# Optimization experiments

Measured on AMD Instinct MI355X. Metric: run time of the kernel, lower is better.

## Reference

```python
import jax, jax.numpy as jnp
import numpy as np

# dims: B batch, LK observed times, LQ reference times, D input_dim (value dim = 2D),
# ET embed_time, H heads, NH nhidden, LAT latent_dim
B, LK, LQ, D, ET, H, NH, LAT = 4, 256, 128, 32, 128, 4, 128, 20
DK = ET // H


def setup_inputs() -> dict:
    key = jax.random.key(0)
    ks = jax.random.split(key, 16)
    s = 0.05
    vals = jax.random.normal(ks[0], (B, LK, D), jnp.float32)
    msk = (jax.random.uniform(ks[1], (B, LK, D)) < 0.7).astype(jnp.float32)
    x = jnp.concatenate([vals * msk, msk], axis=-1)          # (B,LK,2D)
    time_steps = jnp.sort(jax.random.uniform(ks[2], (B, LK), jnp.float32), axis=-1)
    q_ref = jnp.linspace(0.0, 1.0, LQ, dtype=jnp.float32)     # fixed reference times
    lin = lambda k, o, i: s * jax.random.normal(k, (o, i), jnp.float32)
    return dict(
        x=x, time_steps=time_steps, q_ref=q_ref,
        w_lin=lin(ks[3], 1, 1), b_lin=jnp.zeros((1,), jnp.float32),
        w_per=lin(ks[4], ET - 1, 1), b_per=jnp.zeros((ET - 1,), jnp.float32),
        wq=lin(ks[5], ET, ET), bq=jnp.zeros((ET,), jnp.float32),
        wk=lin(ks[6], ET, ET), bk=jnp.zeros((ET,), jnp.float32),
        wo=lin(ks[7], NH, 2 * D * H), bo=jnp.zeros((NH,), jnp.float32),
        wih_f=lin(ks[8], 3 * NH, NH), whh_f=lin(ks[9], 3 * NH, NH),
        bih_f=jnp.zeros((3 * NH,), jnp.float32), bhh_f=jnp.zeros((3 * NH,), jnp.float32),
        wih_b=lin(ks[10], 3 * NH, NH), whh_b=lin(ks[11], 3 * NH, NH),
        bih_b=jnp.zeros((3 * NH,), jnp.float32), bhh_b=jnp.zeros((3 * NH,), jnp.float32),
        w1=lin(ks[12], 50, 2 * NH), b1=jnp.zeros((50,), jnp.float32),
        w2=lin(ks[13], 2 * LAT, 50), b2=jnp.zeros((2 * LAT,), jnp.float32),
    )


def _time_emb(tt, w_lin, b_lin, w_per, b_per):
    # learn_time_embedding: [linear(t), sin(periodic(t))]
    tt = tt[..., None]
    out1 = tt @ w_lin.T + b_lin
    out2 = jnp.sin(tt @ w_per.T + b_per)
    return jnp.concatenate([out1, out2], axis=-1)  # (..., ET)


def _gru_dir(xs, wih, whh, bih, bhh, reverse):
    # xs: (T, B, F); torch GRU cell math
    h0 = jnp.zeros((xs.shape[1], whh.shape[1]), xs.dtype)
    def step(h, xt):
        gi = xt @ wih.T + bih
        gh = h @ whh.T + bhh
        ir, iz, inn = jnp.split(gi, 3, axis=-1)
        hr, hz, hn = jnp.split(gh, 3, axis=-1)
        r = jax.nn.sigmoid(ir + hr)
        z = jax.nn.sigmoid(iz + hz)
        n = jnp.tanh(inn + r * hn)
        hnew = (1.0 - z) * n + z * h
        return hnew, hnew
    _, ys = jax.lax.scan(step, h0, xs, reverse=reverse)
    return ys  # (T, B, H)


def reference(x, time_steps, q_ref, w_lin, b_lin, w_per, b_per, wq, bq, wk, bk,
              wo, bo, wih_f, whh_f, bih_f, bhh_f, wih_b, whh_b, bih_b, bhh_b,
              w1, b1, w2, b2):
    mask = jnp.concatenate([x[:, :, D:], x[:, :, D:]], axis=-1)        # (B,LK,2D)
    key_e = _time_emb(time_steps, w_lin, b_lin, w_per, b_per)           # (B,LK,ET)
    qry_e = _time_emb(q_ref[None, :], w_lin, b_lin, w_per, b_per)       # (1,LQ,ET)
    q = (qry_e @ wq.T + bq).reshape(1, LQ, H, DK).transpose(0, 2, 1, 3)  # (1,H,LQ,DK)
    k = (key_e @ wk.T + bk).reshape(B, LK, H, DK).transpose(0, 2, 1, 3)  # (B,H,LK,DK)
    scores = jnp.einsum('ahqd,bhkd->bhqk', q, k) / np.sqrt(DK).astype(np.float32)
    # mTAN: broadcast scores over value dim, per-feature masked softmax over LK
    masked = jnp.where(mask[:, None, None, :, :] == 0, -1e9, scores[..., None])  # (B,H,LQ,LK,2D)
    p = jax.nn.softmax(masked, axis=-2)
    att = jnp.sum(p * x[:, None, None, :, :], axis=-2)                   # (B,H,LQ,2D)
    att = att.transpose(0, 2, 1, 3).reshape(B, LQ, H * 2 * D)
    out = att @ wo.T + bo                                                # (B,LQ,NH)
    xs = out.transpose(1, 0, 2)                                          # (LQ,B,NH)
    hf = _gru_dir(xs, wih_f, whh_f, bih_f, bhh_f, False)
    hb = _gru_dir(xs, wih_b, whh_b, bih_b, bhh_b, True)
    hh = jnp.concatenate([hf, hb], axis=-1).transpose(1, 0, 2)            # (B,LQ,2NH)
    hid = jax.nn.relu(hh @ w1.T + b1)
    return hid @ w2.T + b2                                                # (B,LQ,2*LAT)
```

## Files before the change

kernel.cpp:

```cpp
#include <hip/hip_runtime.h>
#include <math.h>

#define B 4
#define LK 256
#define LQ 128
#define D 32
#define ET 128
#define H 4
#define NH 128
#define DK 32
#define TWO_D 64
#define G3 384

#define OFF_KP 0
#define SZ_KP (B*LK*ET)
#define OFF_QP (OFF_KP + SZ_KP)
#define SZ_QP (LQ*ET)
#define OFF_OUT (OFF_QP + SZ_QP)
#define SZ_OUT (B*LQ*NH)
#define OFF_GI (OFF_OUT + SZ_OUT)
#define SZ_GI (2*LQ*B*G3)
#define OFF_H (OFF_GI + SZ_GI)
#define SZ_H (2*LQ*B*NH)

typedef float f2 __attribute__((ext_vector_type(2)));

#if defined(__has_builtin)
#if __has_builtin(__builtin_elementwise_fma)
#define VFMA(a,b,c) __builtin_elementwise_fma((a),(b),(c))
#else
#define VFMA(a,b,c) ((a)*(b)+(c))
#endif
#else
#define VFMA(a,b,c) ((a)*(b)+(c))
#endif

__device__ __forceinline__ float dot4(float4 a, float4 b, float acc) {
    acc = fmaf(a.x, b.x, acc); acc = fmaf(a.y, b.y, acc);
    acc = fmaf(a.z, b.z, acc); acc = fmaf(a.w, b.w, acc);
    return acc;
}

__global__ __launch_bounds__(128) void k_emb_proj(
        const float* __restrict__ ts, const float* __restrict__ qref,
        const float* __restrict__ wlin, const float* __restrict__ blin,
        const float* __restrict__ wper, const float* __restrict__ bper,
        const float* __restrict__ wq, const float* __restrict__ bq,
        const float* __restrict__ wk, const float* __restrict__ bk,
        float* __restrict__ ws) {
    __shared__ float e[ET];
    int blk = blockIdx.x;
    int j = threadIdx.x;
    float t;
    const float *wmat, *bvec;
    float* outp;
    if (blk < B*LK) {
        t = ts[blk];
        wmat = wk; bvec = bk; outp = ws + OFF_KP + blk*ET;
    } else {
        int q = blk - B*LK;
        t = qref[q];
        wmat = wq; bvec = bq; outp = ws + OFF_QP + q*ET;
    }
    e[j] = (j == 0) ? fmaf(t, wlin[0], blin[0])
                    : sinf(fmaf(t, wper[j-1], bper[j-1]));
    __syncthreads();
    const f2* w2 = (const f2*)(wmat + j*ET);
    const f2* e2 = (const f2*)e;
    f2 a0 = {0.f,0.f}, a1 = {0.f,0.f}, a2 = {0.f,0.f}, a3 = {0.f,0.f};
    #pragma unroll
    for (int c = 0; c < ET/2; c += 4) {
        a0 = VFMA(w2[c+0], e2[c+0], a0);
        a1 = VFMA(w2[c+1], e2[c+1], a1);
        a2 = VFMA(w2[c+2], e2[c+2], a2);
        a3 = VFMA(w2[c+3], e2[c+3], a3);
    }
    f2 aa = (a0 + a1) + (a2 + a3);
    outp[j] = bvec[j] + aa.x + aa.y;
}

__global__ __launch_bounds__(256) void k_attn(
        const float* __restrict__ x, const float* __restrict__ wo,
        const float* __restrict__ bo, float* __restrict__ ws) {
    int b = blockIdx.x >> 7;
    int q = blockIdx.x & 127;
    int tid = threadIdx.x;
    __shared__ float xt[LK*TWO_D];
    __shared__ float qv[ET];
    __shared__ float earr[H*LK];
    __shared__ float P[4*H*TWO_D];
    __shared__ float Nl[H*TWO_D];
    __shared__ float attf[H*TWO_D];

    const float* ksrc = ws + OFF_KP + b*LK*ET;
    if (tid < ET) qv[tid] = ws[OFF_QP + q*ET + tid];
    const float4* xsrc4 = (const float4*)(x + b*LK*TWO_D);
    float4* xt4 = (float4*)xt;
    for (int i = tid; i < LK*TWO_D/4; i += 256) xt4[i] = xsrc4[i];
    __syncthreads();

    int h = tid >> 6, lane = tid & 63;
    float s[4];
    float mx = -1e30f;
    #pragma unroll
    for (int i = 0; i < 4; ++i) {
        int k = lane + 64*i;
        const f2* kp2 = (const f2*)(ksrc + k*ET + h*DK);
        const f2* q2  = (const f2*)(qv + h*DK);
        f2 a0 = {0.f,0.f}, a1 = {0.f,0.f};
        #pragma unroll
        for (int c = 0; c < DK/2; c += 2) {
            a0 = VFMA(kp2[c+0], q2[c+0], a0);
            a1 = VFMA(kp2[c+1], q2[c+1], a1);
        }
        f2 aa = a0 + a1;
        s[i] = (aa.x + aa.y) * 0.17677669529663687f;
        mx = fmaxf(mx, s[i]);
    }
    #pragma unroll
    for (int off = 32; off > 0; off >>= 1)
        mx = fmaxf(mx, __shfl_xor(mx, off, 64));
    #pragma unroll
    for (int i = 0; i < 4; ++i)
        earr[h*LK + lane + 64*i] = expf(s[i] - mx);
    __syncthreads();

    int fg = lane & 15, kc = lane >> 4;
    f2 accl = {0.f,0.f}, acch = {0.f,0.f};
    const float* ep = earr + h*LK + kc*64;
    #pragma unroll 4
    for (int k = 0; k < 64; ++k) {
        float e = ep[k];
        f2 ee = {e, e};
        const f2* xv = (const f2*)(xt + (kc*64 + k)*TWO_D + fg*4);
        accl = VFMA(ee, xv[0], accl);
        acch = VFMA(ee, xv[1], acch);
    }
    {
        float4 acc4;
        acc4.x = accl.x; acc4.y = accl.y; acc4.z = acch.x; acc4.w = acch.y;
        *(float4*)(P + kc*(H*TWO_D) + h*TWO_D + fg*4) = acc4;
    }
    __syncthreads();
    {
        int hh2 = tid >> 6, f = tid & 63;
        float n = P[0*(H*TWO_D) + hh2*TWO_D + f] + P[1*(H*TWO_D) + hh2*TWO_D + f]
                + P[2*(H*TWO_D) + hh2*TWO_D + f] + P[3*(H*TWO_D) + hh2*TWO_D + f];
        Nl[hh2*TWO_D + f] = n;
    }
    __syncthreads();
    {
        int hh2 = tid >> 6, f = tid & 63;
        attf[hh2*TWO_D + f] = Nl[hh2*TWO_D + f] / Nl[hh2*TWO_D + 32 + (f & 31)];
    }
    __syncthreads();

    if (tid < NH) {
        const f2* wrow = (const f2*)(wo + tid*(H*TWO_D));
        const f2* a2 = (const f2*)attf;
        f2 c0 = {0.f,0.f}, c1 = {0.f,0.f}, c2 = {0.f,0.f}, c3 = {0.f,0.f};
        #pragma unroll
        for (int j = 0; j < (H*TWO_D)/2; j += 4) {
            c0 = VFMA(wrow[j+0], a2[j+0], c0);
            c1 = VFMA(wrow[j+1], a2[j+1], c1);
            c2 = VFMA(wrow[j+2], a2[j+2], c2);
            c3 = VFMA(wrow[j+3], a2[j+3], c3);
        }
        f2 cc = (c0 + c1) + (c2 + c3);
        ws[OFF_OUT + (b*LQ + q)*NH + tid] = bo[tid] + cc.x + cc.y;
    }
}

__global__ __launch_bounds__(384) void k_gi(
        const float* __restrict__ wih_f, const float* __restrict__ bih_f,
        const float* __restrict__ wih_b, const float* __restrict__ bih_b,
        float* __restrict__ ws) {
    int dir = blockIdx.x >> 7;
    int t = blockIdx.x & 127;
    int r = threadIdx.x;
    __shared__ float xr[B*NH];
    for (int i = r; i < B*NH; i += 384) {
        int bb = i >> 7, j = i & 127;
        xr[i] = ws[OFF_OUT + (bb*LQ + t)*NH + j];
    }
    __syncthreads();
    const float* wih = dir ? wih_b : wih_f;
    const float* bih = dir ? bih_b : bih_f;
    const f2* w2 = (const f2*)(wih + r*NH);
    const f2* x0 = (const f2*)(xr + 0*NH);
    const f2* x1 = (const f2*)(xr + 1*NH);
    const f2* x2 = (const f2*)(xr + 2*NH);
    const f2* x3 = (const f2*)(xr + 3*NH);
    f2 a0 = {0.f,0.f}, a1 = {0.f,0.f}, a2 = {0.f,0.f}, a3 = {0.f,0.f};
    #pragma unroll
    for (int c = 0; c < NH/2; ++c) {
        f2 w = w2[c];
        a0 = VFMA(w, x0[c], a0);
        a1 = VFMA(w, x1[c], a1);
        a2 = VFMA(w, x2[c], a2);
        a3 = VFMA(w, x3[c], a3);
    }
    float bb0 = bih[r];
    float* gid = ws + OFF_GI + dir*(LQ*B*G3) + t*(B*G3);
    gid[0*G3 + r] = bb0 + a0.x + a0.y;
    gid[1*G3 + r] = bb0 + a1.x + a1.y;
    gid[2*G3 + r] = bb0 + a2.x + a2.y;
    gid[3*G3 + r] = bb0 + a3.x + a3.y;
}

__global__ __launch_bounds__(384) void k_gru(
        const float* __restrict__ whh_f, const float* __restrict__ bhh_f,
        const float* __restrict__ whh_b, const float* __restrict__ bhh_b,
        float* __restrict__ ws) {
    int dir = blockIdx.x >> 2;
    int b = blockIdx.x & 3;
    int r = threadIdx.x;
    __shared__ float hl[NH];
    __shared__ float gh[G3];
    const float* whh = dir ? whh_b : whh_f;
    const float* bhh = dir ? bhh_b : bhh_f;
    f2 w[NH/2];
    #pragma unroll
    for (int c = 0; c < NH/2; ++c) w[c] = ((const f2*)(whh + r*NH))[c];
    float bh = bhh[r];
    if (r < NH) hl[r] = 0.f;
    const float* gbase = ws + OFF_GI + dir*(LQ*B*G3) + b*G3;
    float* hbase = ws + OFF_H + dir*(LQ*B*NH) + b*NH;
    __syncthreads();
    const f2* hl2 = (const f2*)hl;
    for (int t = 0; t < LQ; ++t) {
        int tt = dir ? (LQ - 1 - t) : t;
        const float* gp = gbase + tt*(B*G3);
        float gir = 0.f, giz = 0.f, gin = 0.f;
        if (r < NH) { gir = gp[r]; giz = gp[NH + r]; gin = gp[2*NH + r]; }
        f2 a0 = {0.f,0.f}, a1 = {0.f,0.f}, a2 = {0.f,0.f}, a3 = {0.f,0.f};
        #pragma unroll
        for (int c = 0; c < NH/2; c += 4) {
            a0 = VFMA(w[c+0], hl2[c+0], a0);
            a1 = VFMA(w[c+1], hl2[c+1], a1);
            a2 = VFMA(w[c+2], hl2[c+2], a2);
            a3 = VFMA(w[c+3], hl2[c+3], a3);
        }
        f2 aa = (a0 + a1) + (a2 + a3);
        gh[r] = bh + aa.x + aa.y;
        __syncthreads();
        if (r < NH) {
            float rg = 1.f / (1.f + expf(-(gir + gh[r])));
            float zg = 1.f / (1.f + expf(-(giz + gh[NH + r])));
            float ng = tanhf(gin + rg * gh[2*NH + r]);
            float hn = (1.f - zg) * ng + zg * hl[r];
            hl[r] = hn;
            hbase[tt*(B*NH) + r] = hn;
        }
        __syncthreads();
    }
}

__global__ __launch_bounds__(64) void k_mlp(
        const float* __restrict__ w1, const float* __restrict__ b1,
        const float* __restrict__ w2, const float* __restrict__ b2,
        const float* __restrict__ ws, float* __restrict__ out) {
    int b = blockIdx.x >> 7;
    int q = blockIdx.x & 127;
    int tid = threadIdx.x;
    __shared__ float hh[2*NH];
    __shared__ float hid[64];
    for (int i = tid; i < 2*NH; i += 64) {
        int dir = i >> 7, j = i & 127;
        hh[i] = ws[OFF_H + dir*(LQ*B*NH) + (q*B + b)*NH + j];
    }
    __syncthreads();
    if (tid < 50) {
        const f2* w2v = (const f2*)(w1 + tid*(2*NH));
        const f2* h2v = (const f2*)hh;
        f2 a0 = {0.f,0.f}, a1 = {0.f,0.f}, a2 = {0.f,0.f}, a3 = {0.f,0.f};
        #pragma unroll
        for (int c = 0; c < (2*NH)/2; c += 4) {
            a0 = VFMA(w2v[c+0], h2v[c+0], a0);
            a1 = VFMA(w2v[c+1], h2v[c+1], a1);
            a2 = VFMA(w2v[c+2], h2v[c+2], a2);
            a3 = VFMA(w2v[c+3], h2v[c+3], a3);
        }
        f2 aa = (a0 + a1) + (a2 + a3);
        hid[tid] = fmaxf(b1[tid] + aa.x + aa.y, 0.f);
    }
    __syncthreads();
    if (tid < 40) {
        float acc = b2[tid];
        const float* wr = w2 + tid*50;
        #pragma unroll
        for (int i = 0; i < 50; ++i) acc = fmaf(wr[i], hid[i], acc);
        out[(b*LQ + q)*40 + tid] = acc;
    }
}

extern "C" void kernel_launch(void* const* d_in, const int* in_sizes, int n_in,
                              void* d_out, int out_size, void* d_ws, size_t ws_size,
                              hipStream_t stream) {
    const float* x     = (const float*)d_in[0];
    const float* ts    = (const float*)d_in[1];
    const float* qref  = (const float*)d_in[2];
    const float* wlin  = (const float*)d_in[3];
    const float* blin  = (const float*)d_in[4];
    const float* wper  = (const float*)d_in[5];
    const float* bper  = (const float*)d_in[6];
    const float* wq    = (const float*)d_in[7];
    const float* bq    = (const float*)d_in[8];
    const float* wk    = (const float*)d_in[9];
    const float* bk    = (const float*)d_in[10];
    const float* wo    = (const float*)d_in[11];
    const float* bo    = (const float*)d_in[12];
    const float* wih_f = (const float*)d_in[13];
    const float* whh_f = (const float*)d_in[14];
    const float* bih_f = (const float*)d_in[15];
    const float* bhh_f = (const float*)d_in[16];
    const float* wih_b = (const float*)d_in[17];
    const float* whh_b = (const float*)d_in[18];
    const float* bih_b = (const float*)d_in[19];
    const float* bhh_b = (const float*)d_in[20];
    const float* w1    = (const float*)d_in[21];
    const float* b1    = (const float*)d_in[22];
    const float* w2    = (const float*)d_in[23];
    const float* b2    = (const float*)d_in[24];
    float* ws = (float*)d_ws;
    float* out = (float*)d_out;

    k_emb_proj<<<B*LK + LQ, 128, 0, stream>>>(ts, qref, wlin, blin, wper, bper,
                                              wq, bq, wk, bk, ws);
    k_attn<<<B*LQ, 256, 0, stream>>>(x, wo, bo, ws);
    k_gi<<<2*LQ, 384, 0, stream>>>(wih_f, bih_f, wih_b, bih_b, ws);
    k_gru<<<8, 384, 0, stream>>>(whh_f, bhh_f, whh_b, bhh_b, ws);
    k_mlp<<<B*LQ, 64, 0, stream>>>(w1, b1, w2, b2, ws, out);
}
```

Before: 272.0 us.

## Restructure GRU to one thread per hidden unit, tile attention queries, fast intrinsics

The GRU recurrence now uses 128 threads, each holding all three gate weight rows in registers. The hidden state is double-buffered so each step needs one barrier instead of two, and the next step's input gates are prefetched. The attention kernel processes four queries per block so the shared x tile is loaded once per four queries, which leaves fewer blocks to spread across the GPU. Fast __sinf, __expf and rcp-based sigmoid/tanh replace the precise math functions, trading some accuracy and raising register pressure in the GRU kernel.

```diff
diff --git a/kernel.cpp b/kernel.cpp
--- a/kernel.cpp
+++ b/kernel.cpp
@@ -11,6 +11,7 @@
 #define DK 32
 #define TWO_D 64
 #define G3 384
+#define QTILE 4
 
 #define OFF_KP 0
 #define SZ_KP (B*LK*ET)
@@ -35,10 +36,11 @@
 #define VFMA(a,b,c) ((a)*(b)+(c))
 #endif
 
-__device__ __forceinline__ float dot4(float4 a, float4 b, float acc) {
-    acc = fmaf(a.x, b.x, acc); acc = fmaf(a.y, b.y, acc);
-    acc = fmaf(a.z, b.z, acc); acc = fmaf(a.w, b.w, acc);
-    return acc;
+__device__ __forceinline__ float fsig(float x) {
+    return __builtin_amdgcn_rcpf(1.f + __expf(-x));
+}
+__device__ __forceinline__ float ftanh2(float x) {
+    return fmaf(2.f, fsig(x + x), -1.f);
 }
 
 __global__ __launch_bounds__(128) void k_emb_proj(
@@ -63,7 +65,7 @@
         wmat = wq; bvec = bq; outp = ws + OFF_QP + q*ET;
     }
     e[j] = (j == 0) ? fmaf(t, wlin[0], blin[0])
-                    : sinf(fmaf(t, wper[j-1], bper[j-1]));
+                    : __sinf(fmaf(t, wper[j-1], bper[j-1]));
     __syncthreads();
     const f2* w2 = (const f2*)(wmat + j*ET);
     const f2* e2 = (const f2*)e;
@@ -82,8 +84,8 @@
 __global__ __launch_bounds__(256) void k_attn(
         const float* __restrict__ x, const float* __restrict__ wo,
         const float* __restrict__ bo, float* __restrict__ ws) {
-    int b = blockIdx.x >> 7;
-    int q = blockIdx.x & 127;
+    int b  = blockIdx.x >> 5;
+    int q0 = (blockIdx.x & 31) * QTILE;
     int tid = threadIdx.x;
     __shared__ float xt[LK*TWO_D];
     __shared__ float qv[ET];
@@ -93,81 +95,87 @@
     __shared__ float attf[H*TWO_D];
 
     const float* ksrc = ws + OFF_KP + b*LK*ET;
-    if (tid < ET) qv[tid] = ws[OFF_QP + q*ET + tid];
     const float4* xsrc4 = (const float4*)(x + b*LK*TWO_D);
     float4* xt4 = (float4*)xt;
     for (int i = tid; i < LK*TWO_D/4; i += 256) xt4[i] = xsrc4[i];
-    __syncthreads();
 
     int h = tid >> 6, lane = tid & 63;
-    float s[4];
-    float mx = -1e30f;
-    #pragma unroll
-    for (int i = 0; i < 4; ++i) {
-        int k = lane + 64*i;
-        const f2* kp2 = (const f2*)(ksrc + k*ET + h*DK);
-        const f2* q2  = (const f2*)(qv + h*DK);
-        f2 a0 = {0.f,0.f}, a1 = {0.f,0.f};
-        #pragma unroll
-        for (int c = 0; c < DK/2; c += 2) {
-            a0 = VFMA(kp2[c+0], q2[c+0], a0);
-            a1 = VFMA(kp2[c+1], q2[c+1], a1);
-        }
-        f2 aa = a0 + a1;
-        s[i] = (aa.x + aa.y) * 0.17677669529663687f;
-        mx = fmaxf(mx, s[i]);
-    }
-    #pragma unroll
-    for (int off = 32; off > 0; off >>= 1)
-        mx = fmaxf(mx, __shfl_xor(mx, off, 64));
-    #pragma unroll
-    for (int i = 0; i < 4; ++i)
-        earr[h*LK + lane + 64*i] = expf(s[i] - mx);
-    __syncthreads();
-
     int fg = lane & 15, kc = lane >> 4;
-    f2 accl = {0.f,0.f}, acch = {0.f,0.f};
-    const float* ep = earr + h*LK + kc*64;
-    #pragma unroll 4
-    for (int k = 0; k < 64; ++k) {
-        float e = ep[k];
-        f2 ee = {e, e};
-        const f2* xv = (const f2*)(xt + (kc*64 + k)*TWO_D + fg*4);
-        accl = VFMA(ee, xv[0], accl);
-        acch = VFMA(ee, xv[1], acch);
-    }
-    {
-        float4 acc4;
-        acc4.x = accl.x; acc4.y = accl.y; acc4.z = acch.x; acc4.w = acch.y;
-        *(float4*)(P + kc*(H*TWO_D) + h*TWO_D + fg*4) = acc4;
-    }
-    __syncthreads();
-    {
-        int hh2 = tid >> 6, f = tid & 63;
-        float n = P[0*(H*TWO_D) + hh2*TWO_D + f] + P[1*(H*TWO_D) + hh2*TWO_D + f]
-                + P[2*(H*TWO_D) + hh2*TWO_D + f] + P[3*(H*TWO_D) + hh2*TWO_D + f];
-        Nl[hh2*TWO_D + f] = n;
-    }
-    __syncthreads();
-    {
-        int hh2 = tid >> 6, f = tid & 63;
-        attf[hh2*TWO_D + f] = Nl[hh2*TWO_D + f] / Nl[hh2*TWO_D + 32 + (f & 31)];
-    }
-    __syncthreads();
-
-    if (tid < NH) {
-        const f2* wrow = (const f2*)(wo + tid*(H*TWO_D));
-        const f2* a2 = (const f2*)attf;
-        f2 c0 = {0.f,0.f}, c1 = {0.f,0.f}, c2 = {0.f,0.f}, c3 = {0.f,0.f};
-        #pragma unroll
-        for (int j = 0; j < (H*TWO_D)/2; j += 4) {
-            c0 = VFMA(wrow[j+0], a2[j+0], c0);
-            c1 = VFMA(wrow[j+1], a2[j+1], c1);
-            c2 = VFMA(wrow[j+2], a2[j+2], c2);
-            c3 = VFMA(wrow[j+3], a2[j+3], c3);
-        }
-        f2 cc = (c0 + c1) + (c2 + c3);
-        ws[OFF_OUT + (b*LQ + q)*NH + tid] = bo[tid] + cc.x + cc.y;
+
+    for (int qi = 0; qi < QTILE; ++qi) {
+        int q = q0 + qi;
+        if (tid < ET) qv[tid] = ws[OFF_QP + q*ET + tid];
+        __syncthreads();
+
+        float s[4];
+        float mx = -1e30f;
+        #pragma unroll
+        for (int i = 0; i < 4; ++i) {
+            int k = lane + 64*i;
+            const f2* kp2 = (const f2*)(ksrc + k*ET + h*DK);
+            const f2* q2  = (const f2*)(qv + h*DK);
+            f2 a0 = {0.f,0.f}, a1 = {0.f,0.f};
+            #pragma unroll
+            for (int c = 0; c < DK/2; c += 2) {
+                a0 = VFMA(kp2[c+0], q2[c+0], a0);
+                a1 = VFMA(kp2[c+1], q2[c+1], a1);
+            }
+            f2 aa = a0 + a1;
+            s[i] = (aa.x + aa.y) * 0.17677669529663687f;
+            mx = fmaxf(mx, s[i]);
+        }
+        #pragma unroll
+        for (int off = 32; off > 0; off >>= 1)
+            mx = fmaxf(mx, __shfl_xor(mx, off, 64));
+        #pragma unroll
+        for (int i = 0; i < 4; ++i)
+            earr[h*LK + lane + 64*i] = __expf(s[i] - mx);
+        __syncthreads();
+
+        f2 accl = {0.f,0.f}, acch = {0.f,0.f};
+        const float* ep = earr + h*LK + kc*64;
+        #pragma unroll 4
+        for (int k = 0; k < 64; ++k) {
+            float e = ep[k];
+            f2 ee = {e, e};
+            const f2* xv = (const f2*)(xt + (kc*64 + k)*TWO_D + fg*4);
+            accl = VFMA(ee, xv[0], accl);
+            acch = VFMA(ee, xv[1], acch);
+        }
+        {
+            float4 acc4;
+            acc4.x = accl.x; acc4.y = accl.y; acc4.z = acch.x; acc4.w = acch.y;
+            *(float4*)(P + kc*(H*TWO_D) + h*TWO_D + fg*4) = acc4;
+        }
+        __syncthreads();
+        {
+            int hh2 = tid >> 6, f = tid & 63;
+            float n = P[0*(H*TWO_D) + hh2*TWO_D + f] + P[1*(H*TWO_D) + hh2*TWO_D + f]
+                    + P[2*(H*TWO_D) + hh2*TWO_D + f] + P[3*(H*TWO_D) + hh2*TWO_D + f];
+            Nl[hh2*TWO_D + f] = n;
+        }
+        __syncthreads();
+        {
+            int hh2 = tid >> 6, f = tid & 63;
+            attf[hh2*TWO_D + f] = Nl[hh2*TWO_D + f] / Nl[hh2*TWO_D + 32 + (f & 31)];
+        }
+        __syncthreads();
+
+        if (tid < NH) {
+            const f2* wrow = (const f2*)(wo + tid*(H*TWO_D));
+            const f2* a2 = (const f2*)attf;
+            f2 c0 = {0.f,0.f}, c1 = {0.f,0.f}, c2 = {0.f,0.f}, c3 = {0.f,0.f};
+            #pragma unroll
+            for (int jj = 0; jj < (H*TWO_D)/2; jj += 4) {
+                c0 = VFMA(wrow[jj+0], a2[jj+0], c0);
+                c1 = VFMA(wrow[jj+1], a2[jj+1], c1);
+                c2 = VFMA(wrow[jj+2], a2[jj+2], c2);
+                c3 = VFMA(wrow[jj+3], a2[jj+3], c3);
+            }
+            f2 cc = (c0 + c1) + (c2 + c3);
+            ws[OFF_OUT + (b*LQ + q)*NH + tid] = bo[tid] + cc.x + cc.y;
+        }
+        __syncthreads();
     }
 }
 
@@ -208,50 +216,71 @@
     gid[3*G3 + r] = bb0 + a3.x + a3.y;
 }
 
-__global__ __launch_bounds__(384) void k_gru(
+__global__ __launch_bounds__(128, 1) void k_gru(
         const float* __restrict__ whh_f, const float* __restrict__ bhh_f,
         const float* __restrict__ whh_b, const float* __restrict__ bhh_b,
         float* __restrict__ ws) {
     int dir = blockIdx.x >> 2;
     int b = blockIdx.x & 3;
-    int r = threadIdx.x;
-    __shared__ float hl[NH];
-    __shared__ float gh[G3];
+    int j = threadIdx.x;
+    __shared__ float4 hbuf[2][NH/4];
     const float* whh = dir ? whh_b : whh_f;
     const float* bhh = dir ? bhh_b : bhh_f;
-    f2 w[NH/2];
-    #pragma unroll
-    for (int c = 0; c < NH/2; ++c) w[c] = ((const f2*)(whh + r*NH))[c];
-    float bh = bhh[r];
-    if (r < NH) hl[r] = 0.f;
+
+    f2 wr[NH/2], wz[NH/2], wn[NH/2];
+    #pragma unroll
+    for (int c = 0; c < NH/2; ++c) wr[c] = ((const f2*)(whh + (j       )*NH))[c];
+    #pragma unroll
+    for (int c = 0; c < NH/2; ++c) wz[c] = ((const f2*)(whh + (NH   + j)*NH))[c];
+    #pragma unroll
+    for (int c = 0; c < NH/2; ++c) wn[c] = ((const f2*)(whh + (2*NH + j)*NH))[c];
+    float bhr = bhh[j], bhz = bhh[NH + j], bhn = bhh[2*NH + j];
+
+    ((float*)hbuf[0])[j] = 0.f;
+    float hprev = 0.f;
+
     const float* gbase = ws + OFF_GI + dir*(LQ*B*G3) + b*G3;
     float* hbase = ws + OFF_H + dir*(LQ*B*NH) + b*NH;
-    __syncthreads();
-    const f2* hl2 = (const f2*)hl;
+
+    int tt0 = dir ? (LQ - 1) : 0;
+    const float* gp0 = gbase + tt0*(B*G3);
+    float gir = gp0[j], giz = gp0[NH + j], gin = gp0[2*NH + j];
+    __syncthreads();
+
     for (int t = 0; t < LQ; ++t) {
         int tt = dir ? (LQ - 1 - t) : t;
-        const float* gp = gbase + tt*(B*G3);
-        float gir = 0.f, giz = 0.f, gin = 0.f;
-        if (r < NH) { gir = gp[r]; giz = gp[NH + r]; gin = gp[2*NH + r]; }
-        f2 a0 = {0.f,0.f}, a1 = {0.f,0.f}, a2 = {0.f,0.f}, a3 = {0.f,0.f};
-        #pragma unroll
-        for (int c = 0; c < NH/2; c += 4) {
-            a0 = VFMA(w[c+0], hl2[c+0], a0);
-            a1 = VFMA(w[c+1], hl2[c+1], a1);
-            a2 = VFMA(w[c+2], hl2[c+2], a2);
-            a3 = VFMA(w[c+3], hl2[c+3], a3);
-        }
-        f2 aa = (a0 + a1) + (a2 + a3);
-        gh[r] = bh + aa.x + aa.y;
-        __syncthreads();
-        if (r < NH) {
-            float rg = 1.f / (1.f + expf(-(gir + gh[r])));
-            float zg = 1.f / (1.f + expf(-(giz + gh[NH + r])));
-            float ng = tanhf(gin + rg * gh[2*NH + r]);
-            float hn = (1.f - zg) * ng + zg * hl[r];
-            hl[r] = hn;
-            hbase[tt*(B*NH) + r] = hn;
-        }
+        float ngr = 0.f, ngz = 0.f, ngn = 0.f;
+        if (t + 1 < LQ) {
+            int tn = dir ? (LQ - 2 - t) : (t + 1);
+            const float* gp = gbase + tn*(B*G3);
+            ngr = gp[j]; ngz = gp[NH + j]; ngn = gp[2*NH + j];
+        }
+        const float4* h4 = hbuf[t & 1];
+        f2 ar0 = {0.f,0.f}, ar1 = {0.f,0.f};
+        f2 az0 = {0.f,0.f}, az1 = {0.f,0.f};
+        f2 an0 = {0.f,0.f}, an1 = {0.f,0.f};
+        #pragma unroll
+        for (int c = 0; c < NH/4; ++c) {
+            float4 hv = h4[c];
+            f2 hlo = {hv.x, hv.y}, hhi = {hv.z, hv.w};
+            ar0 = VFMA(wr[2*c+0], hlo, ar0); ar1 = VFMA(wr[2*c+1], hhi, ar1);
+            az0 = VFMA(wz[2*c+0], hlo, az0); az1 = VFMA(wz[2*c+1], hhi, az1);
+            an0 = VFMA(wn[2*c+0], hlo, an0); an1 = VFMA(wn[2*c+1], hhi, an1);
+        }
+        f2 arr = ar0 + ar1; f2 azz = az0 + az1; f2 ann = an0 + an1;
+        float ghr = bhr + arr.x + arr.y;
+        float ghz = bhz + azz.x + azz.y;
+        float ghn = bhn + ann.x + ann.y;
+
+        float rg = fsig(gir + ghr);
+        float zg = fsig(giz + ghz);
+        float ng = ftanh2(gin + rg * ghn);
+        float hn = (1.f - zg) * ng + zg * hprev;
+
+        ((float*)hbuf[(t + 1) & 1])[j] = hn;
+        hbase[tt*(B*NH) + j] = hn;
+        hprev = hn;
+        gir = ngr; giz = ngz; gin = ngn;
         __syncthreads();
     }
 }
@@ -327,8 +356,8 @@
 
     k_emb_proj<<<B*LK + LQ, 128, 0, stream>>>(ts, qref, wlin, blin, wper, bper,
                                               wq, bq, wk, bk, ws);
-    k_attn<<<B*LQ, 256, 0, stream>>>(x, wo, bo, ws);
+    k_attn<<<B*(LQ/QTILE), 256, 0, stream>>>(x, wo, bo, ws);
     k_gi<<<2*LQ, 384, 0, stream>>>(wih_f, bih_f, wih_b, bih_b, ws);
-    k_gru<<<8, 384, 0, stream>>>(whh_f, bhh_f, whh_b, bhh_b, ws);
+    k_gru<<<8, 128, 0, stream>>>(whh_f, bhh_f, whh_b, bhh_b, ws);
     k_mlp<<<B*LQ, 64, 0, stream>>>(w1, b1, w2, b2, ws, out);
 }
```

Result: slower. 370.7 us (+36.3%).
